# Performance work log

Measured on AMD Instinct MI355X. Metric: run time of the kernel, lower is better.

## Reference

```python
import jax, jax.numpy as jnp
import numpy as np

ENC_DIM, DEC_DIM, ATT_DIM = 2048, 512, 512
B, L = 64, 1024


def setup_inputs() -> dict:
    key = jax.random.key(0)
    ks = jax.random.split(key, 8)
    s_enc = 1.0 / np.sqrt(ENC_DIM)
    s_dec = 1.0 / np.sqrt(DEC_DIM)
    s_att = 1.0 / np.sqrt(ATT_DIM)
    return {
        "encoder_out": jax.random.normal(ks[0], (B, L, ENC_DIM), jnp.float32),
        "decoder_hidden": jax.random.normal(ks[1], (B, DEC_DIM), jnp.float32),
        "W_enc": jax.random.uniform(ks[2], (ENC_DIM, ATT_DIM), jnp.float32, -s_enc, s_enc),
        "b_enc": jax.random.uniform(ks[3], (ATT_DIM,), jnp.float32, -s_enc, s_enc),
        "W_dec": jax.random.uniform(ks[4], (DEC_DIM, ATT_DIM), jnp.float32, -s_dec, s_dec),
        "b_dec": jax.random.uniform(ks[5], (ATT_DIM,), jnp.float32, -s_dec, s_dec),
        "W_full": jax.random.uniform(ks[6], (ATT_DIM,), jnp.float32, -s_att, s_att),
        "b_full": jax.random.uniform(ks[7], (), jnp.float32, -s_att, s_att),
    }


def reference(encoder_out, decoder_hidden, W_enc, b_enc, W_dec, b_dec, W_full, b_full):
    # att1: [B, L, A]
    att1 = jnp.einsum('ble,ea->bla', encoder_out, W_enc) + b_enc
    # att2: [B, A]
    att2 = decoder_hidden @ W_dec + b_dec
    # scores: [B, L]
    att = jnp.einsum('bla,a->bl', jnp.tanh(att1 + att2[:, None, :]), W_full) + b_full
    alpha = jax.nn.softmax(att, axis=1)
    # NOTE: faithful to source -- weighted sum is over att1, not encoder_out.
    attention_weighted_encoding = jnp.einsum('bla,bl->ba', att1, alpha)
    return attention_weighted_encoding, alpha
```

## Files before the change

### kernel.cpp

```cpp
#include <hip/hip_runtime.h>
#include <hip/hip_bf16.h>


#define Bn 64
#define Ln 1024
#define En 2048
#define An 512
#define TM 64
#define NTILES (Ln/TM)
#define AWE_OFF 0
#define ALPHA_OFF (Bn*An)

using short8 = __attribute__((ext_vector_type(8))) short;
using sh4    = __attribute__((ext_vector_type(4))) short;
using f32x4  = __attribute__((ext_vector_type(4))) float;

__device__ inline short f2bf(float x){
    unsigned u = __builtin_bit_cast(unsigned, x);
    unsigned r = (u + 0x7fffu + ((u >> 16) & 1u)) >> 16;
    return (short)r;
}
__device__ inline float tanh_fast(float x){
    return 2.0f * __frcp_rn(1.0f + __expf(-2.0f * x)) - 1.0f;
}

__global__ __launch_bounds__(256) void k_pack(const float* __restrict__ W,
                                              unsigned short* __restrict__ Wp){
    int t = blockIdx.x * 256 + threadIdx.x;
    int f = t >> 6, lane = t & 63;
    int kb = f >> 5, nc = f & 31;
    int k0 = kb * 32 + (lane >> 4) * 8;
    int col = nc * 16 + (lane & 15);
    short8 v;
#pragma unroll
    for (int j = 0; j < 8; ++j)
        v[j] = f2bf(W[(size_t)(k0 + j) * An + col]);
    *(short8*)(Wp + (size_t)f * 512 + lane * 8) = v;
}

__global__ __launch_bounds__(256) void k_att2(const float* __restrict__ dh,
                                              const float* __restrict__ Wd,
                                              const float* __restrict__ bd,
                                              float* __restrict__ att2){
    int b = blockIdx.x, tid = threadIdx.x;
    __shared__ float dl[512];
    dl[tid]       = dh[b * 512 + tid];
    dl[tid + 256] = dh[b * 512 + tid + 256];
    __syncthreads();
    for (int a = tid; a < An; a += 256){
        float s = bd[a];
        for (int k = 0; k < 512; ++k)
            s = fmaf(dl[k], Wd[(size_t)k * An + a], s);
        att2[b * An + a] = s;
    }
}


#define MFMA(a, b, c) __builtin_amdgcn_mfma_f32_16x16x32_bf16((a), (b), (c), 0, 0, 0)

#define PHASE(P, AB0, AB1, NXT, RC, RN)                                       \
{                                                                             \
    __syncthreads();                                                          \
    const unsigned short* bp = Bbase + (P) * 32768;                           \
    short8 bf00 = *(const short8*)(bp);                                       \
    short8 bf01 = *(const short8*)(bp + 512);                                 \
    short8 bf10 = *(const short8*)(bp + 16384);                               \
    short8 bf11 = *(const short8*)(bp + 16384 + 512);                         \
    if ((P) + 2 < 32)                                                         \
        RN = *(const float4*)(apt + ((P) + 2) * 64);                          \
    if ((P) + 1 < 32){                                                        \
        sh4 sv;                                                               \
        sv[0] = f2bf(RC.x); sv[1] = f2bf(RC.y);                               \
        sv[2] = f2bf(RC.z); sv[3] = f2bf(RC.w);                               \
        *(sh4*)((NXT) + sbyte) = sv;                                          \
    }                                                                         \
    _Pragma("unroll")                                                         \
    for (int mi = 0; mi < 4; ++mi){                                           \
        short8 af0 = *(const short8*)((AB0) + mi * 2048);                     \
        short8 af1 = *(const short8*)((AB1) + mi * 2048);                     \
        acc[mi][0] = MFMA(af0, bf00, acc[mi][0]);                             \
        acc[mi][1] = MFMA(af0, bf01, acc[mi][1]);                             \
        acc[mi][0] = MFMA(af1, bf10, acc[mi][0]);                             \
        acc[mi][1] = MFMA(af1, bf11, acc[mi][1]);                             \
    }                                                                         \
}

__global__ __launch_bounds__(1024)
void k_main(const float* __restrict__ enc, const unsigned short* __restrict__ Wp,
            const float* __restrict__ benc, const float* __restrict__ att2,
            const float* __restrict__ wfull, float* __restrict__ out,
            float* __restrict__ pawe_ws, float* __restrict__ ms_ws){
    const int wg   = blockIdx.x;
    const int b    = wg >> 4;
    const int tile = wg & 15;
    const int l0   = tile * TM;
    const int tid  = threadIdx.x;
    const int lane = tid & 63, w = tid >> 6;

    __shared__ alignas(16) unsigned short Alds0[TM * 64];
    __shared__ alignas(16) unsigned short Alds1[TM * 64];
    __shared__ float red[16][TM];
    __shared__ float plds[TM];
    char* const alds0 = (char*)Alds0;
    char* const alds1 = (char*)Alds1;

    f32x4 acc[4][2];
#pragma unroll
    for (int mi = 0; mi < 4; ++mi)
#pragma unroll
        for (int ni = 0; ni < 2; ++ni)
            acc[mi][ni] = (f32x4){0.f, 0.f, 0.f, 0.f};

    const int srow  = tid >> 4;
    const int sbyte = srow * 128 + (((tid & 15) * 8) ^ ((srow & 7) << 4));
    const float* apt = enc + ((size_t)(b * Ln + l0 + srow)) * En + (tid & 15) * 4;

    const unsigned short* Bbase = Wp + (size_t)(w * 2) * 512 + lane * 8;

    const int arow = lane & 15;
    const int akb  = (lane >> 4) * 16;
    const int sw   = (arow & 7) << 4;
    const int off0 = akb ^ sw;
    const int off1 = (64 + akb) ^ sw;
    const char* a0s0 = alds0 + arow * 128 + off0;
    const char* a0s1 = alds0 + arow * 128 + off1;
    const char* a1s0 = alds1 + arow * 128 + off0;
    const char* a1s1 = alds1 + arow * 128 + off1;

    float4 rc = *(const float4*)(apt);
    {
        sh4 sv;
        sv[0] = f2bf(rc.x); sv[1] = f2bf(rc.y); sv[2] = f2bf(rc.z); sv[3] = f2bf(rc.w);
        *(sh4*)(alds0 + sbyte) = sv;
    }
    rc = *(const float4*)(apt + 64);
    float4 rn = rc;

    for (int p = 0; p < 32; p += 2){
        PHASE(p,     a0s0, a0s1, alds1, rc, rn)
        PHASE(p + 1, a1s0, a1s1, alds0, rn, rc)
    }

    float be[2], a2[2], wfv[2];
    const int cbase = w * 32 + (lane & 15);
#pragma unroll
    for (int ni = 0; ni < 2; ++ni){
        int c = cbase + ni * 16;
        be[ni]  = benc[c];
        a2[ni]  = att2[b * An + c];
        wfv[ni] = wfull[c];
    }

    float tsum[4][4];
#pragma unroll
    for (int mi = 0; mi < 4; ++mi)
#pragma unroll
        for (int j = 0; j < 4; ++j)
            tsum[mi][j] = 0.f;
#pragma unroll
    for (int mi = 0; mi < 4; ++mi)
#pragma unroll
        for (int ni = 0; ni < 2; ++ni)
#pragma unroll
            for (int j = 0; j < 4; ++j){
                float vv = acc[mi][ni][j] + be[ni];
                acc[mi][ni][j] = vv;
                tsum[mi][j] += tanh_fast(vv + a2[ni]) * wfv[ni];
            }

#pragma unroll
    for (int mi = 0; mi < 4; ++mi)
#pragma unroll
        for (int j = 0; j < 4; ++j){
            float t = tsum[mi][j];
            t += __shfl_xor(t, 1); t += __shfl_xor(t, 2);
            t += __shfl_xor(t, 4); t += __shfl_xor(t, 8);
            if ((lane & 15) == 0)
                red[w][mi * 16 + (lane >> 4) * 4 + j] = t;
        }
    __syncthreads();

    if (tid < 64){
        float s = 0.f;
#pragma unroll
        for (int k = 0; k < 16; ++k)
            s += red[k][tid];
        out[ALPHA_OFF + b * Ln + l0 + tid] = s;
        float m = s;
        m = fmaxf(m, __shfl_xor(m, 1));  m = fmaxf(m, __shfl_xor(m, 2));
        m = fmaxf(m, __shfl_xor(m, 4));  m = fmaxf(m, __shfl_xor(m, 8));
        m = fmaxf(m, __shfl_xor(m, 16)); m = fmaxf(m, __shfl_xor(m, 32));
        float pv = __expf(s - m);
        float sm = pv;
        sm += __shfl_xor(sm, 1);  sm += __shfl_xor(sm, 2);
        sm += __shfl_xor(sm, 4);  sm += __shfl_xor(sm, 8);
        sm += __shfl_xor(sm, 16); sm += __shfl_xor(sm, 32);
        plds[tid] = pv;
        if (tid == 0){ ms_ws[wg * 2] = m; ms_ws[wg * 2 + 1] = sm; }
    }
    __syncthreads();

    float pp0 = 0.f, pp1 = 0.f;
#pragma unroll
    for (int mi = 0; mi < 4; ++mi)
#pragma unroll
        for (int j = 0; j < 4; ++j){
            float pr = plds[mi * 16 + (lane >> 4) * 4 + j];
            pp0 += pr * acc[mi][0][j];
            pp1 += pr * acc[mi][1][j];
        }
    pp0 += __shfl_xor(pp0, 16); pp0 += __shfl_xor(pp0, 32);
    pp1 += __shfl_xor(pp1, 16); pp1 += __shfl_xor(pp1, 32);
    if (lane < 16){
        pawe_ws[(size_t)wg * An + w * 32 + lane]      = pp0;
        pawe_ws[(size_t)wg * An + w * 32 + 16 + lane] = pp1;
    }
}

__global__ __launch_bounds__(256) void k_final(const float* __restrict__ pawe,
                                               const float* __restrict__ ms,
                                               float* __restrict__ out){
    int b = blockIdx.x, tid = threadIdx.x;
    __shared__ float scale[NTILES];
    __shared__ float sh[2];
    if (tid < 64){
        int lane = tid;
        float m = -1e30f, su = 0.f;
        if (lane < NTILES){ m = ms[(b * NTILES + lane) * 2]; su = ms[(b * NTILES + lane) * 2 + 1]; }
        float mm = m;
        mm = fmaxf(mm, __shfl_xor(mm, 1)); mm = fmaxf(mm, __shfl_xor(mm, 2));
        mm = fmaxf(mm, __shfl_xor(mm, 4)); mm = fmaxf(mm, __shfl_xor(mm, 8));
        float sc = (lane < NTILES) ? su * __expf(m - mm) : 0.f;
        float tot = sc;
        tot += __shfl_xor(tot, 1); tot += __shfl_xor(tot, 2);
        tot += __shfl_xor(tot, 4); tot += __shfl_xor(tot, 8);
        if (lane < NTILES) scale[lane] = __expf(m - mm);
        if (lane == 0){ sh[0] = 1.0f / tot; sh[1] = mm; }
    }
    __syncthreads();
    float inv = sh[0], mm = sh[1];
    for (int a = tid; a < An; a += 256){
        float s = 0.f;
#pragma unroll
        for (int t = 0; t < NTILES; ++t)
            s += pawe[((size_t)(b * NTILES + t)) * An + a] * scale[t];
        out[AWE_OFF + b * An + a] = s * inv;
    }
    for (int l = tid; l < Ln; l += 256){
        float s = out[ALPHA_OFF + b * Ln + l];
        out[ALPHA_OFF + b * Ln + l] = __expf(s - mm) * inv;
    }
}

extern "C" void kernel_launch(void* const* d_in, const int* in_sizes, int n_in,
                              void* d_out, int out_size, void* d_ws, size_t ws_size,
                              hipStream_t stream){
    const float* enc   = (const float*)d_in[0];
    const float* dh    = (const float*)d_in[1];
    const float* Wenc  = (const float*)d_in[2];
    const float* benc  = (const float*)d_in[3];
    const float* Wdec  = (const float*)d_in[4];
    const float* bdec  = (const float*)d_in[5];
    const float* wfull = (const float*)d_in[6];
    float* out = (float*)d_out;

    char* ws = (char*)d_ws;
    unsigned short* Wp = (unsigned short*)ws;
    float* att2 = (float*)(ws + (2u << 20));
    float* pawe = (float*)(ws + (2u << 20) + (128u << 10));
    float* msb  = (float*)(ws + (4u << 20) + (128u << 10));

    k_pack<<<512, 256, 0, stream>>>(Wenc, Wp);
    k_att2<<<Bn, 256, 0, stream>>>(dh, Wdec, bdec, att2);
    k_main<<<Bn * NTILES, 1024, 0, stream>>>(enc, Wp, benc, att2, wfull, out, pawe, msb);
    k_final<<<Bn, 256, 0, stream>>>(pawe, msb, out);
}
```

Baseline: 289.7 us.

## Use four-slot LDS ring with barrier every two k-steps; merge prep kernels

The main GEMM loop moves from a double-buffered LDS scheme with one barrier per k-step to a four-slot ring. Two k-tiles are staged at a time, so a barrier is needed only every two k-steps, and the global loads for the next two tiles are issued ahead. Separately, the weight-packing and att2 kernels are merged into one launch to save a kernel launch. This uses more LDS and more registers in flight, which could reduce occupancy or add load latency at the tail, where clamped indices cause redundant loads.

```diff
diff --git a/kernel.cpp b/kernel.cpp
--- a/kernel.cpp
+++ b/kernel.cpp
@@ -10,6 +10,7 @@
 #define NTILES (Ln/TM)
 #define AWE_OFF 0
 #define ALPHA_OFF (Bn*An)
+#define TILEB 8192
 
 using short8 = __attribute__((ext_vector_type(8))) short;
 using sh4    = __attribute__((ext_vector_type(4))) short;
@@ -24,66 +25,65 @@
     return 2.0f * __frcp_rn(1.0f + __expf(-2.0f * x)) - 1.0f;
 }
 
-__global__ __launch_bounds__(256) void k_pack(const float* __restrict__ W,
-                                              unsigned short* __restrict__ Wp){
-    int t = blockIdx.x * 256 + threadIdx.x;
-    int f = t >> 6, lane = t & 63;
-    int kb = f >> 5, nc = f & 31;
-    int k0 = kb * 32 + (lane >> 4) * 8;
-    int col = nc * 16 + (lane & 15);
-    short8 v;
-#pragma unroll
-    for (int j = 0; j < 8; ++j)
-        v[j] = f2bf(W[(size_t)(k0 + j) * An + col]);
-    *(short8*)(Wp + (size_t)f * 512 + lane * 8) = v;
-}
-
-__global__ __launch_bounds__(256) void k_att2(const float* __restrict__ dh,
+__global__ __launch_bounds__(256) void k_prep(const float* __restrict__ W,
+                                              unsigned short* __restrict__ Wp,
+                                              const float* __restrict__ dh,
                                               const float* __restrict__ Wd,
                                               const float* __restrict__ bd,
                                               float* __restrict__ att2){
-    int b = blockIdx.x, tid = threadIdx.x;
     __shared__ float dl[512];
-    dl[tid]       = dh[b * 512 + tid];
-    dl[tid + 256] = dh[b * 512 + tid + 256];
-    __syncthreads();
-    for (int a = tid; a < An; a += 256){
-        float s = bd[a];
-        for (int k = 0; k < 512; ++k)
-            s = fmaf(dl[k], Wd[(size_t)k * An + a], s);
-        att2[b * An + a] = s;
+    int blk = blockIdx.x, tid = threadIdx.x;
+    if (blk < 512){
+        int t = blk * 256 + tid;
+        int f = t >> 6, lane = t & 63;
+        int kb = f >> 5, nc = f & 31;
+        int k0 = kb * 32 + (lane >> 4) * 8;
+        int col = nc * 16 + (lane & 15);
+        short8 v;
+#pragma unroll
+        for (int j = 0; j < 8; ++j)
+            v[j] = f2bf(W[(size_t)(k0 + j) * An + col]);
+        *(short8*)(Wp + (size_t)f * 512 + lane * 8) = v;
+    } else {
+        int b = blk - 512;
+        dl[tid]       = dh[b * 512 + tid];
+        dl[tid + 256] = dh[b * 512 + tid + 256];
+        __syncthreads();
+        for (int a = tid; a < An; a += 256){
+            float s = bd[a];
+            for (int k = 0; k < 512; ++k)
+                s = fmaf(dl[k], Wd[(size_t)k * An + a], s);
+            att2[b * An + a] = s;
+        }
     }
 }
 
 
 #define MFMA(a, b, c) __builtin_amdgcn_mfma_f32_16x16x32_bf16((a), (b), (c), 0, 0, 0)
 
-#define PHASE(P, AB0, AB1, NXT, RC, RN)                                       \
-{                                                                             \
-    __syncthreads();                                                          \
-    const unsigned short* bp = Bbase + (P) * 32768;                           \
+#define BLOAD(P)                                                              \
+    const unsigned short* bp = Bbase + (size_t)(P) * 32768;                   \
     short8 bf00 = *(const short8*)(bp);                                       \
     short8 bf01 = *(const short8*)(bp + 512);                                 \
     short8 bf10 = *(const short8*)(bp + 16384);                               \
-    short8 bf11 = *(const short8*)(bp + 16384 + 512);                         \
-    if ((P) + 2 < 32)                                                         \
-        RN = *(const float4*)(apt + ((P) + 2) * 64);                          \
-    if ((P) + 1 < 32){                                                        \
-        sh4 sv;                                                               \
-        sv[0] = f2bf(RC.x); sv[1] = f2bf(RC.y);                               \
-        sv[2] = f2bf(RC.z); sv[3] = f2bf(RC.w);                               \
-        *(sh4*)((NXT) + sbyte) = sv;                                          \
-    }                                                                         \
+    short8 bf11 = *(const short8*)(bp + 16384 + 512);
+
+#define STAGE(Q, R)                                                           \
+    { sh4 sv;                                                                 \
+      sv[0] = f2bf(R.x); sv[1] = f2bf(R.y);                                   \
+      sv[2] = f2bf(R.z); sv[3] = f2bf(R.w);                                   \
+      *(sh4*)(swp + (Q) * TILEB) = sv; }
+
+#define MFMAS(Q)                                                              \
     _Pragma("unroll")                                                         \
     for (int mi = 0; mi < 4; ++mi){                                           \
-        short8 af0 = *(const short8*)((AB0) + mi * 2048);                     \
-        short8 af1 = *(const short8*)((AB1) + mi * 2048);                     \
+        short8 af0 = *(const short8*)(as0 + (Q) * TILEB + mi * 2048);         \
+        short8 af1 = *(const short8*)(as1 + (Q) * TILEB + mi * 2048);         \
         acc[mi][0] = MFMA(af0, bf00, acc[mi][0]);                             \
         acc[mi][1] = MFMA(af0, bf01, acc[mi][1]);                             \
         acc[mi][0] = MFMA(af1, bf10, acc[mi][0]);                             \
         acc[mi][1] = MFMA(af1, bf11, acc[mi][1]);                             \
-    }                                                                         \
-}
+    }
 
 __global__ __launch_bounds__(1024)
 void k_main(const float* __restrict__ enc, const unsigned short* __restrict__ Wp,
@@ -97,12 +97,10 @@
     const int tid  = threadIdx.x;
     const int lane = tid & 63, w = tid >> 6;
 
-    __shared__ alignas(16) unsigned short Alds0[TM * 64];
-    __shared__ alignas(16) unsigned short Alds1[TM * 64];
+    __shared__ alignas(16) unsigned short Alds[4][TM * 64];
     __shared__ float red[16][TM];
     __shared__ float plds[TM];
-    char* const alds0 = (char*)Alds0;
-    char* const alds1 = (char*)Alds1;
+    char* const alds = (char*)Alds;
 
     f32x4 acc[4][2];
 #pragma unroll
@@ -113,6 +111,7 @@
 
     const int srow  = tid >> 4;
     const int sbyte = srow * 128 + (((tid & 15) * 8) ^ ((srow & 7) << 4));
+    char* const swp = alds + sbyte;
     const float* apt = enc + ((size_t)(b * Ln + l0 + srow)) * En + (tid & 15) * 4;
 
     const unsigned short* Bbase = Wp + (size_t)(w * 2) * 512 + lane * 8;
@@ -120,25 +119,47 @@
     const int arow = lane & 15;
     const int akb  = (lane >> 4) * 16;
     const int sw   = (arow & 7) << 4;
-    const int off0 = akb ^ sw;
-    const int off1 = (64 + akb) ^ sw;
-    const char* a0s0 = alds0 + arow * 128 + off0;
-    const char* a0s1 = alds0 + arow * 128 + off1;
-    const char* a1s0 = alds1 + arow * 128 + off0;
-    const char* a1s1 = alds1 + arow * 128 + off1;
-
-    float4 rc = *(const float4*)(apt);
-    {
-        sh4 sv;
-        sv[0] = f2bf(rc.x); sv[1] = f2bf(rc.y); sv[2] = f2bf(rc.z); sv[3] = f2bf(rc.w);
-        *(sh4*)(alds0 + sbyte) = sv;
-    }
-    rc = *(const float4*)(apt + 64);
-    float4 rn = rc;
-
-    for (int p = 0; p < 32; p += 2){
-        PHASE(p,     a0s0, a0s1, alds1, rc, rn)
-        PHASE(p + 1, a1s0, a1s1, alds0, rn, rc)
+    const char* const as0 = alds + arow * 128 + (akb ^ sw);
+    const char* const as1 = alds + arow * 128 + ((64 + akb) ^ sw);
+
+    float4 ra = *(const float4*)(apt);
+    float4 rb = *(const float4*)(apt + 64);
+    STAGE(0, ra)
+    STAGE(1, rb)
+    ra = *(const float4*)(apt + 2 * 64);
+    rb = *(const float4*)(apt + 3 * 64);
+
+    for (int p = 0; p < 32; p += 4){
+        __syncthreads();
+        {
+            BLOAD(p)
+            STAGE(2, ra)
+            STAGE(3, rb)
+            int t0 = p + 4 > 31 ? 31 : p + 4;
+            int t1 = p + 5 > 31 ? 31 : p + 5;
+            ra = *(const float4*)(apt + t0 * 64);
+            rb = *(const float4*)(apt + t1 * 64);
+            MFMAS(0)
+        }
+        {
+            BLOAD(p + 1)
+            MFMAS(1)
+        }
+        __syncthreads();
+        {
+            BLOAD(p + 2)
+            STAGE(0, ra)
+            STAGE(1, rb)
+            int t0 = p + 6 > 31 ? 31 : p + 6;
+            int t1 = p + 7 > 31 ? 31 : p + 7;
+            ra = *(const float4*)(apt + t0 * 64);
+            rb = *(const float4*)(apt + t1 * 64);
+            MFMAS(2)
+        }
+        {
+            BLOAD(p + 3)
+            MFMAS(3)
+        }
     }
 
     float be[2], a2[2], wfv[2];
@@ -270,8 +291,7 @@
     float* pawe = (float*)(ws + (2u << 20) + (128u << 10));
     float* msb  = (float*)(ws + (4u << 20) + (128u << 10));
 
-    k_pack<<<512, 256, 0, stream>>>(Wenc, Wp);
-    k_att2<<<Bn, 256, 0, stream>>>(dh, Wdec, bdec, att2);
+    k_prep<<<576, 256, 0, stream>>>(Wenc, Wp, dh, Wdec, bdec, att2);
     k_main<<<Bn * NTILES, 1024, 0, stream>>>(enc, Wp, benc, att2, wfull, out, pawe, msb);
     k_final<<<Bn, 256, 0, stream>>>(pawe, msb, out);
 }
```

New measurement: 253.6 us. 1.14x faster.
